# Kernel tuning notes

Hardware: AMD Instinct MI355X
Metric: run time of the kernel (lower is better)

The kernel has to match this reference:

```python
import jax, jax.numpy as jnp
import numpy as np

NUM_ITER = 3
SLOT_DIM = 16
INPUT_DIM = 256
HIDDEN_DIM = 128
EPS = 1e-8
LN_EPS = 1e-5  # torch LayerNorm default


def _layernorm(x, w, b):
    mu = jnp.mean(x, axis=-1, keepdims=True)
    var = jnp.mean((x - mu) ** 2, axis=-1, keepdims=True)
    return (x - mu) * jax.lax.rsqrt(var + LN_EPS) * w + b


def setup_inputs() -> dict:
    key = jax.random.key(0)
    ks = jax.random.split(key, 12)
    B, N, K = 32, 4096, 8
    D, S, H = INPUT_DIM, SLOT_DIM, HIDDEN_DIM
    inputs = jax.random.normal(ks[0], (B, N, D), dtype=jnp.float32)
    init_slots = jax.random.normal(ks[1], (B, K, S), dtype=jnp.float32)
    return {
        "inputs": inputs,
        "init_slots": init_slots,
        "ln_in_w": jnp.ones((D,), jnp.float32),
        "ln_in_b": jnp.zeros((D,), jnp.float32),
        "ln_s_w": jnp.ones((S,), jnp.float32),
        "ln_s_b": jnp.zeros((S,), jnp.float32),
        "ln_m_w": jnp.ones((S,), jnp.float32),
        "ln_m_b": jnp.zeros((S,), jnp.float32),
        "wq": jax.random.normal(ks[2], (S, S), jnp.float32) * (S ** -0.5),
        "wk": jax.random.normal(ks[3], (S, D), jnp.float32) * (D ** -0.5),
        "wv": jax.random.normal(ks[4], (S, D), jnp.float32) * (D ** -0.5),
        "w_ih": jax.random.normal(ks[5], (3 * S, S), jnp.float32) * (S ** -0.5),
        "w_hh": jax.random.normal(ks[6], (3 * S, S), jnp.float32) * (S ** -0.5),
        "b_ih": jnp.zeros((3 * S,), jnp.float32),
        "b_hh": jnp.zeros((3 * S,), jnp.float32),
        "mlp_w1": jax.random.normal(ks[7], (H, S), jnp.float32) * (S ** -0.5),
        "mlp_b1": jnp.zeros((H,), jnp.float32),
        "mlp_w2": jax.random.normal(ks[8], (S, H), jnp.float32) * (H ** -0.5),
        "mlp_b2": jnp.zeros((S,), jnp.float32),
    }


def _gru_cell(x, h, w_ih, w_hh, b_ih, b_hh):
    # torch GRUCell: gates ordered [r, z, n]
    gi = x @ w_ih.T + b_ih            # [BK, 3S]
    gh = h @ w_hh.T + b_hh
    i_r, i_z, i_n = jnp.split(gi, 3, axis=-1)
    h_r, h_z, h_n = jnp.split(gh, 3, axis=-1)
    r = jax.nn.sigmoid(i_r + h_r)
    z = jax.nn.sigmoid(i_z + h_z)
    n = jnp.tanh(i_n + r * h_n)
    return (1.0 - z) * n + z * h


def reference(inputs, init_slots, ln_in_w, ln_in_b, ln_s_w, ln_s_b, ln_m_w, ln_m_b,
              wq, wk, wv, w_ih, w_hh, b_ih, b_hh, mlp_w1, mlp_b1, mlp_w2, mlp_b2):
    B, N, _ = inputs.shape
    K = init_slots.shape[1]
    scale = SLOT_DIM ** -0.5

    x = _layernorm(inputs, ln_in_w, ln_in_b)
    k = jnp.einsum('bnd,sd->bns', x, wk)   # [B,N,S]
    v = jnp.einsum('bnd,sd->bns', x, wv)

    slots = init_slots
    attn = None
    for _ in range(NUM_ITER):
        slots_prev = slots
        q = jnp.einsum('bks,ts->bkt', _layernorm(slots, ln_s_w, ln_s_b), wq)
        logits = jnp.einsum('bks,bns->bkn', q, k) * scale       # [B,K,N]
        attn = jax.nn.softmax(logits, axis=1) + EPS              # softmax over SLOTS
        attn = attn / jnp.sum(attn, axis=-1, keepdims=True)
        updates = jnp.einsum('bkn,bns->bks', attn, v)            # [B,K,S]
        h = _gru_cell(updates.reshape(B * K, -1), slots_prev.reshape(B * K, -1),
                      w_ih, w_hh, b_ih, b_hh).reshape(B, K, -1)
        y = _layernorm(h, ln_m_w, ln_m_b)
        mlp = jax.nn.relu(y @ mlp_w1.T + mlp_b1) @ mlp_w2.T + mlp_b2
        slots = h + mlp
    return slots, attn
```

## Files before the change

kernel.cpp:

```cpp
#include <hip/hip_runtime.h>
#include <cstddef>


typedef unsigned short ushort_t;
typedef __attribute__((ext_vector_type(8))) short short8;
typedef __attribute__((ext_vector_type(4))) float f32x4;

__device__ __forceinline__ float sigmoid_f(float x){ return 1.f/(1.f+__expf(-x)); }
__device__ __forceinline__ float tanh_f(float x){ return 1.f - 2.f/(__expf(2.f*x)+1.f); }

__device__ __forceinline__ ushort_t f2bf(float x){
  unsigned u = __float_as_uint(x);
  return (ushort_t)((u + 0x7FFFu + ((u>>16)&1u)) >> 16);
}
__device__ __forceinline__ float bf2f(ushort_t b){
  return __uint_as_float(((unsigned)b) << 16);
}
__device__ __forceinline__ void split_bf(float v, short& hi, short& lo){
  unsigned u = __float_as_uint(v);
  hi = (short)(u >> 16);
  float hf = __uint_as_float(u & 0xFFFF0000u);
  lo = (short)(__float_as_uint(v - hf) >> 16);
}

__device__ __forceinline__ unsigned ld_cohpt(const unsigned* p){
  unsigned v;
  asm volatile("global_load_dword %0, %1, off sc0 sc1\n\t"
               "s_waitcnt vmcnt(0)"
               : "=v"(v) : "v"(p) : "memory");
  return v;
}
__device__ __forceinline__ void st_agent(float* p, float v){
  __hip_atomic_store(p, v, __ATOMIC_RELAXED, __HIP_MEMORY_SCOPE_AGENT);
}
__device__ __forceinline__ float ld_agent(const float* p){
  return __hip_atomic_load(p, __ATOMIC_RELAXED, __HIP_MEMORY_SCOPE_AGENT);
}

#define VT_OFF    0
#define QS_OFF    16896
#define SLOTS_OFF 17408
#define APART_OFF 17920
#define ULDS_OFF  18048
#define MT_OFF    18560
#define X_OFF     18816
#define KLDS_OFF  (X_OFF + 33792)
#define PT_OFF    X_OFF
#define GW_OFF    (X_OFF + 8448)
#define SMEM_BYTES (X_OFF + 51200)

__global__ __launch_bounds__(256, 2) void k_mega(
    const float* __restrict__ x,
    const float* __restrict__ wk, const float* __restrict__ wv,
    const float* __restrict__ lnw, const float* __restrict__ lnb,
    const float* __restrict__ init_slots,
    float* __restrict__ updp, float* __restrict__ Asum,
    unsigned* __restrict__ barp,
    float* __restrict__ slots_out, float* __restrict__ attn_out,
    const float* __restrict__ w_ih, const float* __restrict__ w_hh,
    const float* __restrict__ b_ih, const float* __restrict__ b_hh,
    const float* __restrict__ mlp_w1, const float* __restrict__ mlp_b1,
    const float* __restrict__ mlp_w2, const float* __restrict__ mlp_b2,
    const float* __restrict__ ln_m_w, const float* __restrict__ ln_m_b,
    const float* __restrict__ ln_s_w, const float* __restrict__ ln_s_b,
    const float* __restrict__ wq)
{
  __shared__ __align__(16) unsigned char smem[SMEM_BYTES];
  ushort_t* vt     = (ushort_t*)(smem + VT_OFF);
  float*    qs     = (float*)(smem + QS_OFF);
  float*    sslots = (float*)(smem + SLOTS_OFF);
  float*    apart  = (float*)(smem + APART_OFF);
  float*    ulds   = (float*)(smem + ULDS_OFF);
  float*    mtf    = (float*)(smem + MT_OFF);
  ushort_t* wlds   = (ushort_t*)(smem + X_OFF);
  float*    klds   = (float*)(smem + KLDS_OFF);
  ushort_t* pt     = (ushort_t*)(smem + PT_OFF);
  float*    s_wih  = (float*)(smem + GW_OFF);
  float*    s_whh  = s_wih + 48*17;
  float*    s_w1   = s_whh + 48*17;
  float*    s_w2   = s_w1 + 128*17;
  float*    s_bih  = s_w2 + 16*129;
  float*    s_bhh  = s_bih + 48;
  float*    s_b1   = s_bhh + 48;
  float*    s_b2   = s_b1 + 128;
  float*    s_lnmw = s_b2 + 16;
  float*    s_lnmb = s_lnmw + 16;
  float*    s_lnsw = s_lnmb + 16;
  float*    s_lnsb = s_lnsw + 16;
  float*    s_wq   = s_lnsb + 16;

  int t = threadIdx.x;
  int lane = t & 63;
  int w = t >> 6;
  int b  = blockIdx.x >> 4;
  int nc = blockIdx.x & 15;
  int n0 = nc << 8;

  {
    unsigned* dst = (unsigned*)wlds;
    #pragma unroll
    for (int i0 = 0; i0 < 8192; i0 += 256) {
      int i = i0 + t;
      int r = i >> 7, ww = i & 127;
      int s = (r & 31);
      int d = ww*2;
      float wa = (s < 16) ? wk[s*256+d]   : wv[(s-16)*256+d];
      float wb = (s < 16) ? wk[s*256+d+1] : wv[(s-16)*256+d+1];
      float w0a = lnw[d]*wa, w0b = lnw[d+1]*wb;
      ushort_t ha = f2bf(w0a), hb2 = f2bf(w0b);
      unsigned word;
      if (r < 32) {
        word = (unsigned)ha | ((unsigned)hb2 << 16);
      } else {
        ushort_t la = f2bf(w0a - bf2f(ha));
        ushort_t lb = f2bf(w0b - bf2f(hb2));
        word = (unsigned)la | ((unsigned)lb << 16);
      }
      dst[r*132 + ww] = word;
    }
  }
  {
    int s = t >> 3, j = t & 7;
    float m = 0.f, tv = 0.f;
    for (int d = j; d < 256; d += 8) {
      float w_ = (s < 16) ? wk[s*256+d] : wv[(s-16)*256+d];
      float w0 = lnw[d]*w_;
      ushort_t hb = f2bf(w0);
      float hf = bf2f(hb);
      float lf = bf2f(f2bf(w0 - hf));
      m  += hf + lf;
      tv  = fmaf(lnb[d], w_, tv);
    }
    m += __shfl_xor(m,1);  m += __shfl_xor(m,2);  m += __shfl_xor(m,4);
    tv += __shfl_xor(tv,1); tv += __shfl_xor(tv,2); tv += __shfl_xor(tv,4);
    if (j == 0) { mtf[s] = m; mtf[32+s] = tv; }
  }
  if (t < 8) {
    float sl[16];
    #pragma unroll
    for (int j2 = 0; j2 < 16; ++j2) sl[j2] = init_slots[(b*8+t)*16+j2];
    float mu = 0.f;
    #pragma unroll
    for (int j2 = 0; j2 < 16; ++j2) mu += sl[j2];
    mu *= (1.f/16.f);
    float var = 0.f;
    #pragma unroll
    for (int j2 = 0; j2 < 16; ++j2) { float d = sl[j2]-mu; var = fmaf(d,d,var); }
    var *= (1.f/16.f);
    float rstd = rsqrtf(var + 1e-5f);
    float y[16];
    #pragma unroll
    for (int j2 = 0; j2 < 16; ++j2) y[j2] = (sl[j2]-mu)*rstd*ln_s_w[j2] + ln_s_b[j2];
    #pragma unroll
    for (int tq = 0; tq < 16; ++tq) {
      float q = 0.f;
      #pragma unroll
      for (int s2 = 0; s2 < 16; ++s2) q = fmaf(y[s2], wq[tq*16+s2], q);
      qs[t*16+tq] = q;
    }
  }
  if (t < 128) sslots[t] = init_slots[b*128 + t];
  __syncthreads();

  int m = lane & 15, quad = lane >> 4;
  const ushort_t* rhk = wlds + (size_t)m*264 + quad*8;
  const ushort_t* rhv = wlds + (size_t)(16+m)*264 + quad*8;
  const ushort_t* rlk = wlds + (size_t)(32+m)*264 + quad*8;
  const ushort_t* rlv = wlds + (size_t)(48+m)*264 + quad*8;
  float mtk  = mtf[m],    mtv  = mtf[16+m];
  float mtkb = mtf[32+m], mtvb = mtf[48+m];

  #pragma unroll
  for (int tile = 0; tile < 4; ++tile) {
    const float* xr = x + (size_t)(b*4096 + n0 + tile*64 + w*16 + m)*256 + quad*8;
    float4 xreg[16];
    #pragma unroll
    for (int kk = 0; kk < 8; ++kk) {
      xreg[2*kk]   = *(const float4*)(xr + kk*32);
      xreg[2*kk+1] = *(const float4*)(xr + kk*32 + 4);
    }
    f32x4 acck = {0.f,0.f,0.f,0.f}, accv = {0.f,0.f,0.f,0.f};
    float sum = 0.f, sumsq = 0.f;
    #pragma unroll
    for (int kk = 0; kk < 8; ++kk) {
      short8 bh_k = *(const short8*)(rhk + kk*32);
      short8 bh_v = *(const short8*)(rhv + kk*32);
      short8 bl_k = *(const short8*)(rlk + kk*32);
      short8 bl_v = *(const short8*)(rlv + kk*32);
      float xv[8] = {xreg[2*kk].x, xreg[2*kk].y, xreg[2*kk].z, xreg[2*kk].w,
                     xreg[2*kk+1].x, xreg[2*kk+1].y, xreg[2*kk+1].z, xreg[2*kk+1].w};
      short8 ah, al;
      #pragma unroll
      for (int j = 0; j < 8; ++j) {
        float v = xv[j];
        sum += v; sumsq = fmaf(v, v, sumsq);
        short h_, l_;
        split_bf(v, h_, l_);
        ah[j] = h_; al[j] = l_;
      }
      acck = __builtin_amdgcn_mfma_f32_16x16x32_bf16(ah, bh_k, acck, 0, 0, 0);
      accv = __builtin_amdgcn_mfma_f32_16x16x32_bf16(ah, bh_v, accv, 0, 0, 0);
      acck = __builtin_amdgcn_mfma_f32_16x16x32_bf16(al, bh_k, acck, 0, 0, 0);
      accv = __builtin_amdgcn_mfma_f32_16x16x32_bf16(al, bh_v, accv, 0, 0, 0);
      acck = __builtin_amdgcn_mfma_f32_16x16x32_bf16(ah, bl_k, acck, 0, 0, 0);
      accv = __builtin_amdgcn_mfma_f32_16x16x32_bf16(ah, bl_v, accv, 0, 0, 0);
    }
    sum   += __shfl_xor(sum, 16);   sum   += __shfl_xor(sum, 32);
    sumsq += __shfl_xor(sumsq, 16); sumsq += __shfl_xor(sumsq, 32);
    #pragma unroll
    for (int r = 0; r < 4; ++r) {
      int row = quad*4 + r;
      float s_ = __shfl(sum,   row);
      float q_ = __shfl(sumsq, row);
      float mu = s_*(1.f/256.f);
      float var = q_*(1.f/256.f) - mu*mu;
      float rstd = rsqrtf(var + 1e-5f);
      float ok = fmaf(rstd, acck[r] - mu*mtk, mtkb);
      float ov = fmaf(rstd, accv[r] - mu*mtv, mtvb);
      int gr = tile*64 + w*16 + row;
      klds[gr*17 + m] = ok;
      short h_, l_;
      split_bf(ov, h_, l_);
      vt[m*264 + gr]      = (ushort_t)h_;
      vt[(16+m)*264 + gr] = (ushort_t)l_;
    }
  }
  __syncthreads();
  float kv[16];
  #pragma unroll
  for (int j = 0; j < 16; ++j) kv[j] = klds[t*17 + j];
  __syncthreads();

  for (int i = t; i < 768; i += 256) {
    int g = i >> 4, j = i & 15;
    s_wih[g*17+j] = w_ih[i];
    s_whh[g*17+j] = w_hh[i];
  }
  for (int i = t; i < 2048; i += 256) {
    int r = i >> 4, c = i & 15;
    s_w1[r*17+c] = mlp_w1[i];
    int r2 = i >> 7, c2 = i & 127;
    s_w2[r2*129+c2] = mlp_w2[i];
  }
  if (t < 48) { s_bih[t] = b_ih[t]; s_bhh[t] = b_hh[t]; }
  if (t < 128) s_b1[t] = mlp_b1[t];
  if (t < 16) {
    s_b2[t] = mlp_b2[t];
    s_lnmw[t] = ln_m_w[t]; s_lnmb[t] = ln_m_b[t];
    s_lnsw[t] = ln_s_w[t]; s_lnsb[t] = ln_s_b[t];
  }
  for (int i = t; i < 256; i += 256) {
    int r = i >> 4, c = i & 15;
    s_wq[r*17+c] = wq[i];
  }
  __syncthreads();

  const short8 z8 = {0,0,0,0,0,0,0,0};
  #pragma unroll 1
  for (int it = 0; it < 3; ++it) {
    float* upd_it = updp + (size_t)(it*32 + b)*2048;
    float* As_it  = Asum + (size_t)(it*32 + b)*128;

    float p8[8];
    {
      float lg[8];
      #pragma unroll
      for (int kk = 0; kk < 8; ++kk) {
        float a = 0.f;
        #pragma unroll
        for (int s = 0; s < 16; ++s) a = fmaf(qs[kk*16+s], kv[s], a);
        lg[kk] = a*0.25f;
      }
      float mx = lg[0];
      #pragma unroll
      for (int kk = 1; kk < 8; ++kk) mx = fmaxf(mx, lg[kk]);
      float se = 0.f;
      #pragma unroll
      for (int kk = 0; kk < 8; ++kk) { lg[kk] = __expf(lg[kk]-mx); se += lg[kk]; }
      float inv = 1.f/se;
      #pragma unroll
      for (int kk = 0; kk < 8; ++kk) p8[kk] = fmaf(lg[kk], inv, 1e-8f);
    }
    #pragma unroll
    for (int kk = 0; kk < 8; ++kk) {
      float r = p8[kk];
      r += __shfl_xor(r, 1);  r += __shfl_xor(r, 2);  r += __shfl_xor(r, 4);
      r += __shfl_xor(r, 8);  r += __shfl_xor(r, 16); r += __shfl_xor(r, 32);
      if (lane == 0) apart[w*8 + kk] = r;
    }
    #pragma unroll
    for (int kk = 0; kk < 8; ++kk) {
      short h_, l_;
      split_bf(p8[kk], h_, l_);
      pt[kk*264 + t]     = (ushort_t)h_;
      pt[(8+kk)*264 + t] = (ushort_t)l_;
    }
    __syncthreads();
    if (t < 8)
      st_agent(As_it + nc*8 + t,
               apart[t] + apart[8+t] + apart[16+t] + apart[24+t]);
    if (w == 0) {
      int mm = lane & 15, q2 = lane >> 4;
      f32x4 acc = {0.f,0.f,0.f,0.f};
      #pragma unroll
      for (int c = 0; c < 8; ++c) {
        int k0 = c*32 + q2*8;
        short8 ah = (mm < 8) ? *(const short8*)&pt[mm*264 + k0]     : z8;
        short8 al = (mm < 8) ? *(const short8*)&pt[(8+mm)*264 + k0] : z8;
        short8 bh = *(const short8*)&vt[mm*264 + k0];
        short8 bl = *(const short8*)&vt[(16+mm)*264 + k0];
        acc = __builtin_amdgcn_mfma_f32_16x16x32_bf16(ah, bh, acc, 0, 0, 0);
        acc = __builtin_amdgcn_mfma_f32_16x16x32_bf16(al, bh, acc, 0, 0, 0);
        acc = __builtin_amdgcn_mfma_f32_16x16x32_bf16(ah, bl, acc, 0, 0, 0);
      }
      int s = lane & 15;
      #pragma unroll
      for (int r = 0; r < 4; ++r) {
        int kk = q2*4 + r;
        if (kk < 8) st_agent(upd_it + nc*128 + kk*16 + s, acc[r]);
      }
    }

    __syncthreads();
    if (t == 0) {
      unsigned* bp = barp + (it*32 + b)*32;
      asm volatile("s_waitcnt vmcnt(0)" ::: "memory");
      atomicAdd(bp, 1u);
      #pragma unroll 1
      for (int spin = 0; spin < (1<<18); ++spin) {
        if (ld_cohpt(bp) >= 16u) break;
        __builtin_amdgcn_s_sleep(8);
      }
    }
    __syncthreads();

    if (t < 8) {
      float a = 0.f;
      #pragma unroll
      for (int nc2 = 0; nc2 < 16; ++nc2) a += ld_agent(As_it + nc2*8 + t);
      apart[t] = a;
    }
    if (t < 128) {
      int bk8 = t >> 4, s = t & 15;
      float us = 0.f;
      #pragma unroll
      for (int nc2 = 0; nc2 < 16; ++nc2)
        us += ld_agent(upd_it + nc2*128 + bk8*16 + s);
      ulds[t] = us;
    }
    __syncthreads();

    if (it == 2) {
      #pragma unroll
      for (int kk = 0; kk < 8; ++kk)
        attn_out[((size_t)(b*8 + kk))*4096 + n0 + t] = p8[kk]*(1.f/apart[kk]);
    }
    if (t < 128 && (it < 2 || nc == 0)) {
      int bk8 = t >> 4, s = t & 15;
      int laneBase = (t & 63) & ~15;
      float invA = 1.f / apart[bk8];
      float u[16], h[16];
      #pragma unroll
      for (int j = 0; j < 16; ++j) {
        u[j] = ulds[bk8*16 + j] * invA;
        h[j] = sslots[bk8*16 + j];
      }
      float hs = h[s];
      float gir = s_bih[s],  giz = s_bih[16+s], gin = s_bih[32+s];
      float ghr = s_bhh[s],  ghz = s_bhh[16+s], ghn = s_bhh[32+s];
      #pragma unroll
      for (int j = 0; j < 16; ++j) {
        gir = fmaf(u[j], s_wih[s*17+j], gir);
        giz = fmaf(u[j], s_wih[(16+s)*17+j], giz);
        gin = fmaf(u[j], s_wih[(32+s)*17+j], gin);
        ghr = fmaf(h[j], s_whh[s*17+j], ghr);
        ghz = fmaf(h[j], s_whh[(16+s)*17+j], ghz);
        ghn = fmaf(h[j], s_whh[(32+s)*17+j], ghn);
      }
      float rr_ = sigmoid_f(gir + ghr);
      float zz = sigmoid_f(giz + ghz);
      float nn = tanh_f(gin + rr_*ghn);
      float hn = (1.f - zz)*nn + zz*hs;

      float ssum = hn;
      #pragma unroll
      for (int mm = 1; mm < 16; mm <<= 1) ssum += __shfl_xor(ssum, mm);
      float mu = ssum*(1.f/16.f);
      float dv = hn - mu;
      float vs = dv*dv;
      #pragma unroll
      for (int mm = 1; mm < 16; mm <<= 1) vs += __shfl_xor(vs, mm);
      float rstd = rsqrtf(vs*(1.f/16.f) + 1e-5f);
      float y = dv*rstd*s_lnmw[s] + s_lnmb[s];

      float yv[16];
      #pragma unroll
      for (int j = 0; j < 16; ++j) yv[j] = __shfl(y, laneBase + j);

      float h1[8];
      #pragma unroll
      for (int i = 0; i < 8; ++i) {
        int jj = i*16 + s;
        float a = s_b1[jj];
        #pragma unroll
        for (int q = 0; q < 16; ++q) a = fmaf(yv[q], s_w1[jj*17+q], a);
        h1[i] = fmaxf(a, 0.f);
      }
      float o = s_b2[s];
      #pragma unroll
      for (int i = 0; i < 8; ++i) {
        #pragma unroll
        for (int sp = 0; sp < 16; ++sp) {
          float hv = __shfl(h1[i], laneBase + sp);
          o = fmaf(hv, s_w2[s*129 + i*16 + sp], o);
        }
      }
      float slot_new = hn + o;
      if (it < 2) {
        sslots[bk8*16 + s] = slot_new;
        float ss = slot_new;
        #pragma unroll
        for (int mm = 1; mm < 16; mm <<= 1) ss += __shfl_xor(ss, mm);
        float mu2 = ss*(1.f/16.f);
        float d2 = slot_new - mu2;
        float v2 = d2*d2;
        #pragma unroll
        for (int mm = 1; mm < 16; mm <<= 1) v2 += __shfl_xor(v2, mm);
        float rstd2 = rsqrtf(v2*(1.f/16.f) + 1e-5f);
        float y2 = d2*rstd2*s_lnsw[s] + s_lnsb[s];
        float qv = 0.f;
        #pragma unroll
        for (int sp = 0; sp < 16; ++sp)
          qv = fmaf(__shfl(y2, laneBase + sp), s_wq[s*17+sp], qv);
        qs[bk8*16 + s] = qv;
      } else {
        slots_out[(b*8 + bk8)*16 + s] = slot_new;
      }
    }
    __syncthreads();
  }
}


__global__ __launch_bounds__(256) void k_prep(
    const float* __restrict__ lnw, const float* __restrict__ lnb,
    const float* __restrict__ wk, const float* __restrict__ wv,
    const float* __restrict__ init_slots,
    const float* __restrict__ ln_s_w, const float* __restrict__ ln_s_b,
    const float* __restrict__ wq,
    ushort_t* __restrict__ Wh, ushort_t* __restrict__ Wl,
    float* __restrict__ mt,
    float* __restrict__ qbuf, float* __restrict__ upd, float* __restrict__ Abuf,
    float* __restrict__ slots_out)
{
  int t = threadIdx.x;
  int i = blockIdx.x*256 + t;
  {
    int s = i >> 8, d = i & 255;
    float w = (s < 16) ? wk[s*256+d] : wv[(s-16)*256+d];
    float w0 = lnw[d]*w;
    ushort_t hb = f2bf(w0);
    ushort_t lb = f2bf(w0 - bf2f(hb));
    Wh[i] = hb; Wl[i] = lb;
  }
  if (blockIdx.x != 0) return;
  {
    int s = t >> 3, j = t & 7;
    float m = 0.f, tv = 0.f;
    for (int d = j; d < 256; d += 8) {
      float w = (s < 16) ? wk[s*256+d] : wv[(s-16)*256+d];
      float w0 = lnw[d]*w;
      ushort_t hb = f2bf(w0);
      float hf = bf2f(hb);
      float lf = bf2f(f2bf(w0 - hf));
      m  += hf + lf;
      tv  = fmaf(lnb[d], w, tv);
    }
    m += __shfl_xor(m,1);  m += __shfl_xor(m,2);  m += __shfl_xor(m,4);
    tv += __shfl_xor(tv,1); tv += __shfl_xor(tv,2); tv += __shfl_xor(tv,4);
    if (j == 0) { mt[s] = m; mt[32+s] = tv; }
  }
  #pragma unroll
  for (int j2 = 0; j2 < 16; ++j2) {
    slots_out[t*16+j2] = init_slots[t*16+j2];
    upd[t*16+j2] = 0.f;
  }
  Abuf[t] = 0.f;
  float sl[16];
  #pragma unroll
  for (int j2 = 0; j2 < 16; ++j2) sl[j2] = init_slots[t*16+j2];
  float mu = 0.f;
  #pragma unroll
  for (int j2 = 0; j2 < 16; ++j2) mu += sl[j2];
  mu *= (1.f/16.f);
  float var = 0.f;
  #pragma unroll
  for (int j2 = 0; j2 < 16; ++j2) { float d = sl[j2]-mu; var = fmaf(d,d,var); }
  var *= (1.f/16.f);
  float rstd = rsqrtf(var + 1e-5f);
  float y[16];
  #pragma unroll
  for (int j2 = 0; j2 < 16; ++j2) y[j2] = (sl[j2]-mu)*rstd*ln_s_w[j2] + ln_s_b[j2];
  #pragma unroll
  for (int tq = 0; tq < 16; ++tq) {
    float q = 0.f;
    #pragma unroll
    for (int s2 = 0; s2 < 16; ++s2) q = fmaf(y[s2], wq[tq*16+s2], q);
    qbuf[t*16+tq] = q;
  }
}

__global__ __launch_bounds__(256, 4) void k_proj(
    const float* __restrict__ x, const ushort_t* __restrict__ Wh,
    const ushort_t* __restrict__ Wl, const float* __restrict__ mt,
    float* __restrict__ kout, float* __restrict__ vout)
{
  __shared__ ushort_t wlds[64*264];
  int t = threadIdx.x;
  int lane = t & 63;
  int p = __builtin_amdgcn_readfirstlane(t >> 6);
  int m = lane & 15, quad = lane >> 4;
  int r0 = blockIdx.x*64;
  {
    const unsigned* srcH = (const unsigned*)Wh;
    const unsigned* srcL = (const unsigned*)Wl;
    unsigned* dst = (unsigned*)wlds;
    #pragma unroll
    for (int i0 = 0; i0 < 8192; i0 += 256) {
      int i = i0 + t;
      int r = i >> 7, w = i & 127;
      unsigned v = (r < 32) ? srcH[r*128 + w] : srcL[(r-32)*128 + w];
      dst[r*132 + w] = v;
    }
  }
  __syncthreads();

  const ushort_t* rhk = wlds + (size_t)m*264 + quad*8;
  const ushort_t* rhv = wlds + (size_t)(16+m)*264 + quad*8;
  const ushort_t* rlk = wlds + (size_t)(32+m)*264 + quad*8;
  const ushort_t* rlv = wlds + (size_t)(48+m)*264 + quad*8;

  const float* xr = x + (size_t)(r0 + p*16 + m)*256 + quad*8;

  f32x4 acck = {0.f,0.f,0.f,0.f}, accv = {0.f,0.f,0.f,0.f};
  float sum = 0.f, sumsq = 0.f;

  #pragma unroll
  for (int kk = 0; kk < 8; ++kk) {
    float4 a0 = *(const float4*)(xr + kk*32);
    float4 a1 = *(const float4*)(xr + kk*32 + 4);
    short8 bh_k = *(const short8*)(rhk + kk*32);
    short8 bh_v = *(const short8*)(rhv + kk*32);
    short8 bl_k = *(const short8*)(rlk + kk*32);
    short8 bl_v = *(const short8*)(rlv + kk*32);
    float xv[8] = {a0.x,a0.y,a0.z,a0.w, a1.x,a1.y,a1.z,a1.w};
    short8 ah, al;
    #pragma unroll
    for (int j = 0; j < 8; ++j) {
      float v = xv[j];
      sum += v; sumsq = fmaf(v, v, sumsq);
      short h_, l_;
      split_bf(v, h_, l_);
      ah[j] = h_; al[j] = l_;
    }
    acck = __builtin_amdgcn_mfma_f32_16x16x32_bf16(ah, bh_k, acck, 0, 0, 0);
    accv = __builtin_amdgcn_mfma_f32_16x16x32_bf16(ah, bh_v, accv, 0, 0, 0);
    acck = __builtin_amdgcn_mfma_f32_16x16x32_bf16(al, bh_k, acck, 0, 0, 0);
    accv = __builtin_amdgcn_mfma_f32_16x16x32_bf16(al, bh_v, accv, 0, 0, 0);
    acck = __builtin_amdgcn_mfma_f32_16x16x32_bf16(ah, bl_k, acck, 0, 0, 0);
    accv = __builtin_amdgcn_mfma_f32_16x16x32_bf16(ah, bl_v, accv, 0, 0, 0);
  }

  sum   += __shfl_xor(sum, 16);  sum   += __shfl_xor(sum, 32);
  sumsq += __shfl_xor(sumsq, 16); sumsq += __shfl_xor(sumsq, 32);

  float mtk  = mt[m],    mtv  = mt[16+m];
  float mtkb = mt[32+m], mtvb = mt[48+m];
  #pragma unroll
  for (int r = 0; r < 4; ++r) {
    int row = quad*4 + r;
    float s_ = __shfl(sum,   row);
    float q_ = __shfl(sumsq, row);
    float mu = s_*(1.f/256.f);
    float var = q_*(1.f/256.f) - mu*mu;
    float rstd = rsqrtf(var + 1e-5f);
    float ok = fmaf(rstd, acck[r] - mu*mtk, mtkb);
    float ov = fmaf(rstd, accv[r] - mu*mtv, mtvb);
    size_t grow = (size_t)(r0 + p*16 + row)*16 + m;
    kout[grow] = ok;
    vout[grow] = ov;
  }
}

__global__ __launch_bounds__(256) void k_attn(
    const float* __restrict__ kproj, const float* __restrict__ vproj,
    const float* __restrict__ qbuf,
    float* __restrict__ upd, float* __restrict__ Abuf,
    float* __restrict__ attn_out, int write_attn)
{
  __shared__ ushort_t vt[32*264];
  __shared__ ushort_t pt[32*264];
  __shared__ float qs[128];
  __shared__ float apart[4][8];
  int b = blockIdx.x >> 4;
  int n0 = (blockIdx.x & 15) * 256;
  int t = threadIdx.x;
  int w = t >> 6, lane = t & 63;

  if (t < 128) qs[t] = qbuf[b*128 + t];

  const float* kr = kproj + ((size_t)(b*4096 + n0 + t))*16;
  const float* vr = vproj + ((size_t)(b*4096 + n0 + t))*16;
  float kv[16], vv[16];
  #pragma unroll
  for (int j = 0; j < 16; j += 4) {
    float4 f = *(const float4*)(kr+j);
    kv[j]=f.x; kv[j+1]=f.y; kv[j+2]=f.z; kv[j+3]=f.w;
    float4 g = *(const float4*)(vr+j);
    vv[j]=g.x; vv[j+1]=g.y; vv[j+2]=g.z; vv[j+3]=g.w;
  }
  #pragma unroll
  for (int s = 0; s < 16; ++s) {
    short h_, l_;
    split_bf(vv[s], h_, l_);
    vt[s*264 + t] = (ushort_t)h_;
    vt[(16+s)*264 + t] = (ushort_t)l_;
  }
  __syncthreads();

  float p8[8];
  {
    float lg[8];
    #pragma unroll
    for (int kk = 0; kk < 8; ++kk) {
      float a = 0.f;
      #pragma unroll
      for (int s = 0; s < 16; ++s) a = fmaf(qs[kk*16+s], kv[s], a);
      lg[kk] = a*0.25f;
    }
    float mx = lg[0];
    #pragma unroll
    for (int kk = 1; kk < 8; ++kk) mx = fmaxf(mx, lg[kk]);
    float se = 0.f;
    #pragma unroll
    for (int kk = 0; kk < 8; ++kk) { lg[kk] = __expf(lg[kk]-mx); se += lg[kk]; }
    float inv = 1.f/se;
    #pragma unroll
    for (int kk = 0; kk < 8; ++kk) {
      float pv = fmaf(lg[kk], inv, 1e-8f);
      p8[kk] = pv;
      if (write_attn) attn_out[((size_t)(b*8+kk))*4096 + n0 + t] = pv;
    }
  }
  #pragma unroll
  for (int kk = 0; kk < 8; ++kk) {
    float r = p8[kk];
    r += __shfl_xor(r, 1);  r += __shfl_xor(r, 2);  r += __shfl_xor(r, 4);
    r += __shfl_xor(r, 8);  r += __shfl_xor(r, 16); r += __shfl_xor(r, 32);
    if (lane == 0) apart[w][kk] = r;
  }
  #pragma unroll
  for (int kk = 0; kk < 8; ++kk) {
    short h_, l_;
    split_bf(p8[kk], h_, l_);
    pt[kk*264 + t] = (ushort_t)h_;
    pt[(16+kk)*264 + t] = (ushort_t)l_;
  }
  __syncthreads();

  if (t < 8)
    atomicAdd(Abuf + b*8 + t,
              apart[0][t] + apart[1][t] + apart[2][t] + apart[3][t]);

  if (w == 0) {
    int mm = lane & 15, quad = lane >> 4;
// ... 169 lines not shown
__global__ __launch_bounds__(256) void k_final(
    float* __restrict__ upd, float* __restrict__ Abuf,
    float* __restrict__ slots, float* __restrict__ qbuf,
    float* __restrict__ attn,
    const float* __restrict__ w_ih, const float* __restrict__ w_hh,
    const float* __restrict__ b_ih, const float* __restrict__ b_hh,
    const float* __restrict__ mlp_w1, const float* __restrict__ mlp_b1,
    const float* __restrict__ mlp_w2, const float* __restrict__ mlp_b2,
    const float* __restrict__ ln_m_w, const float* __restrict__ ln_m_b,
    const float* __restrict__ ln_s_w, const float* __restrict__ ln_s_b,
    const float* __restrict__ wq)
{
  int t = threadIdx.x;
  {
    int bk = blockIdx.x;
    float inv = 1.f / Abuf[bk];
    float4* p = (float4*)(attn + (size_t)bk*4096);
    #pragma unroll 4
    for (int i = t; i < 1024; i += 256) {
      float4 v = p[i];
      v.x *= inv; v.y *= inv; v.z *= inv; v.w *= inv;
      p[i] = v;
    }
  }
  if (blockIdx.x >= 16) return;
  GRU_STAGE_LDS()
  int bk = blockIdx.x*16 + (t >> 4);
  int s = t & 15;
  int laneBase = (t & 63) & ~15;
  gru_body(bk, s, laneBase, 0, upd, Abuf, slots, qbuf,
           s_wih, s_whh, s_bih, s_bhh, s_w1, s_b1, s_w2, s_b2,
           s_lnmw, s_lnmb, s_lnsw, s_lnsb, s_wq);
}

extern "C" void kernel_launch(void* const* d_in, const int* in_sizes, int n_in,
                              void* d_out, int out_size, void* d_ws, size_t ws_size,
                              hipStream_t stream)
{
  const float* inputs     = (const float*)d_in[0];
  const float* init_slots = (const float*)d_in[1];
  const float* ln_in_w    = (const float*)d_in[2];
  const float* ln_in_b    = (const float*)d_in[3];
  const float* ln_s_w     = (const float*)d_in[4];
  const float* ln_s_b     = (const float*)d_in[5];
  const float* ln_m_w     = (const float*)d_in[6];
  const float* ln_m_b     = (const float*)d_in[7];
  const float* wq         = (const float*)d_in[8];
  const float* wk         = (const float*)d_in[9];
  const float* wv         = (const float*)d_in[10];
  const float* w_ih       = (const float*)d_in[11];
  const float* w_hh       = (const float*)d_in[12];
  const float* b_ih       = (const float*)d_in[13];
  const float* b_hh       = (const float*)d_in[14];
  const float* mlp_w1     = (const float*)d_in[15];
  const float* mlp_b1     = (const float*)d_in[16];
  const float* mlp_w2     = (const float*)d_in[17];
  const float* mlp_b2     = (const float*)d_in[18];

  float* ws = (float*)d_ws;
  unsigned* barp = (unsigned*)ws;
  float* updp = ws + 3072;
  float* Asum = ws + 3072 + 196608;
  float* lg    = ws + 211968;
  ushort_t* Wh = (ushort_t*)lg;
  ushort_t* Wl = (ushort_t*)(lg + 4096);
  float* mt    = lg + 8192;
  float* qbuf  = lg + 8320;
  float* upd   = lg + 12416;
  float* Abuf  = lg + 16512;
  float* kproj = lg + 16768;
  float* vproj = kproj + 2097152;

  float* out   = (float*)d_out;
  float* slots = out;
  float* attn  = out + 4096;

  static int s_mode = -1;
  if (s_mode < 0) {
    int dev = 0;
    (void)hipGetDevice(&dev);
    int ncu = 0;
    (void)hipDeviceGetAttribute(&ncu, hipDeviceAttributeMultiprocessorCount, dev);
    int nb = 0;
    if (hipOccupancyMaxActiveBlocksPerMultiprocessor(&nb, (const void*)k_mega,
                                                     256, 0) != hipSuccess)
      nb = 0;
    s_mode = (nb > 0 && ncu > 0 && (long)nb * ncu >= 512) ? 0 : 1;
  }

  if (s_mode == 0) {
    (void)hipMemsetAsync(barp, 0, 3*32*32*sizeof(unsigned), stream);
    k_mega<<<512, 256, 0, stream>>>(inputs, wk, wv, ln_in_w, ln_in_b,
                                    init_slots, updp, Asum, barp, slots, attn,
                                    w_ih, w_hh, b_ih, b_hh,
                                    mlp_w1, mlp_b1, mlp_w2, mlp_b2,
                                    ln_m_w, ln_m_b, ln_s_w, ln_s_b, wq);
    return;
  }

  {
    (void)hipMemsetAsync(barp, 0, 3*32*32*sizeof(unsigned), stream);
    void* kargs[] = {
      (void*)&inputs, (void*)&wk, (void*)&wv, (void*)&ln_in_w, (void*)&ln_in_b,
      (void*)&init_slots, (void*)&updp, (void*)&Asum, (void*)&barp,
      (void*)&slots, (void*)&attn, (void*)&w_ih, (void*)&w_hh,
      (void*)&b_ih, (void*)&b_hh, (void*)&mlp_w1, (void*)&mlp_b1,
      (void*)&mlp_w2, (void*)&mlp_b2, (void*)&ln_m_w, (void*)&ln_m_b,
      (void*)&ln_s_w, (void*)&ln_s_b, (void*)&wq };
    hipError_t err = hipLaunchCooperativeKernel((const void*)k_mega,
                                                dim3(512), dim3(256),
                                                kargs, 0, stream);
    if (err == hipSuccess) return;
    (void)hipGetLastError();
  }

  k_prep<<<32, 256, 0, stream>>>(ln_in_w, ln_in_b, wk, wv, init_slots,
                                 ln_s_w, ln_s_b, wq,
                                 Wh, Wl, mt, qbuf, upd, Abuf, slots);
  k_proj<<<2048, 256, 0, stream>>>(inputs, Wh, Wl, mt, kproj, vproj);
  for (int it = 0; it < 3; ++it) {
    int last = (it == 2);
    k_attn<<<512, 256, 0, stream>>>(kproj, vproj, qbuf, upd, Abuf, attn, last);
    if (!last)
      k_gru<<<16, 256, 0, stream>>>(upd, Abuf, slots, qbuf,
                                    w_ih, w_hh, b_ih, b_hh,
                                    mlp_w1, mlp_b1, mlp_w2, mlp_b2,
                                    ln_m_w, ln_m_b, ln_s_w, ln_s_b, wq);
  }
  k_final<<<256, 256, 0, stream>>>(upd, Abuf, slots, qbuf, attn,
                                   w_ih, w_hh, b_ih, b_hh,
                                   mlp_w1, mlp_b1, mlp_w2, mlp_b2,
                                   ln_m_w, ln_m_b, ln_s_w, ln_s_b, wq);
}
```

Baseline: 307.9 us.

## Split projection out of persistent megakernel into separate prep and proj kernels

The persistent megakernel no longer computes the LayerNorm plus K/V projection itself. Separate k_prep and k_proj kernels now run first, and a slimmer k_iter kernel reads the projected K/V back from global memory, with less LDS per block so three blocks fit per CU instead of two. The barrier memset is folded into k_prep, and the spin timeout is shortened. This trades an extra round trip of K/V through global memory and an extra launch for better occupancy and full-GPU parallelism on the projection.

New measurement: 324.8 us. 1.05x slower.

```diff
diff --git a/kernel.cpp b/kernel.cpp
--- a/kernel.cpp
+++ b/kernel.cpp
@@ -37,23 +37,170 @@
   return __hip_atomic_load(p, __ATOMIC_RELAXED, __HIP_MEMORY_SCOPE_AGENT);
 }
 
-#define VT_OFF    0
-#define QS_OFF    16896
-#define SLOTS_OFF 17408
-#define APART_OFF 17920
-#define ULDS_OFF  18048
-#define MT_OFF    18560
-#define X_OFF     18816
-#define KLDS_OFF  (X_OFF + 33792)
-#define PT_OFF    X_OFF
-#define GW_OFF    (X_OFF + 8448)
-#define SMEM_BYTES (X_OFF + 51200)
-
-__global__ __launch_bounds__(256, 2) void k_mega(
-    const float* __restrict__ x,
+__global__ __launch_bounds__(256) void k_prep(
+    const float* __restrict__ lnw, const float* __restrict__ lnb,
     const float* __restrict__ wk, const float* __restrict__ wv,
-    const float* __restrict__ lnw, const float* __restrict__ lnb,
     const float* __restrict__ init_slots,
+    const float* __restrict__ ln_s_w, const float* __restrict__ ln_s_b,
+    const float* __restrict__ wq,
+    ushort_t* __restrict__ Wh, ushort_t* __restrict__ Wl,
+    float* __restrict__ mt,
+    float* __restrict__ qbuf, float* __restrict__ upd, float* __restrict__ Abuf,
+    unsigned* __restrict__ barp,
+    float* __restrict__ slots_out)
+{
+  int t = threadIdx.x;
+  int i = blockIdx.x*256 + t;
+  {
+    int s = i >> 8, d = i & 255;
+    float w = (s < 16) ? wk[s*256+d] : wv[(s-16)*256+d];
+    float w0 = lnw[d]*w;
+    ushort_t hb = f2bf(w0);
+    ushort_t lb = f2bf(w0 - bf2f(hb));
+    Wh[i] = hb; Wl[i] = lb;
+  }
+  if (blockIdx.x != 0) return;
+  {
+    int s = t >> 3, j = t & 7;
+    float m = 0.f, tv = 0.f;
+    for (int d = j; d < 256; d += 8) {
+      float w = (s < 16) ? wk[s*256+d] : wv[(s-16)*256+d];
+      float w0 = lnw[d]*w;
+      ushort_t hb = f2bf(w0);
+      float hf = bf2f(hb);
+      float lf = bf2f(f2bf(w0 - hf));
+      m  += hf + lf;
+      tv  = fmaf(lnb[d], w, tv);
+    }
+    m += __shfl_xor(m,1);  m += __shfl_xor(m,2);  m += __shfl_xor(m,4);
+    tv += __shfl_xor(tv,1); tv += __shfl_xor(tv,2); tv += __shfl_xor(tv,4);
+    if (j == 0) { mt[s] = m; mt[32+s] = tv; }
+  }
+  #pragma unroll
+  for (int j2 = 0; j2 < 16; ++j2) {
+    slots_out[t*16+j2] = init_slots[t*16+j2];
+    upd[t*16+j2] = 0.f;
+  }
+  Abuf[t] = 0.f;
+  for (int i2 = t; i2 < 3072; i2 += 256) barp[i2] = 0u;
+  float sl[16];
+  #pragma unroll
+  for (int j2 = 0; j2 < 16; ++j2) sl[j2] = init_slots[t*16+j2];
+  float mu = 0.f;
+  #pragma unroll
+  for (int j2 = 0; j2 < 16; ++j2) mu += sl[j2];
+  mu *= (1.f/16.f);
+  float var = 0.f;
+  #pragma unroll
+  for (int j2 = 0; j2 < 16; ++j2) { float d = sl[j2]-mu; var = fmaf(d,d,var); }
+  var *= (1.f/16.f);
+  float rstd = rsqrtf(var + 1e-5f);
+  float y[16];
+  #pragma unroll
+  for (int j2 = 0; j2 < 16; ++j2) y[j2] = (sl[j2]-mu)*rstd*ln_s_w[j2] + ln_s_b[j2];
+  #pragma unroll
+  for (int tq = 0; tq < 16; ++tq) {
+    float q = 0.f;
+    #pragma unroll
+    for (int s2 = 0; s2 < 16; ++s2) q = fmaf(y[s2], wq[tq*16+s2], q);
+    qbuf[t*16+tq] = q;
+  }
+}
+
+__global__ __launch_bounds__(256, 4) void k_proj(
+    const float* __restrict__ x, const ushort_t* __restrict__ Wh,
+    const ushort_t* __restrict__ Wl, const float* __restrict__ mt,
+    float* __restrict__ kout, float* __restrict__ vout)
+{
+  __shared__ ushort_t wlds[64*264];
+  int t = threadIdx.x;
+  int lane = t & 63;
+  int p = __builtin_amdgcn_readfirstlane(t >> 6);
+  int m = lane & 15, quad = lane >> 4;
+  int r0 = blockIdx.x*64;
+  {
+    const unsigned* srcH = (const unsigned*)Wh;
+    const unsigned* srcL = (const unsigned*)Wl;
+    unsigned* dst = (unsigned*)wlds;
+    #pragma unroll
+    for (int i0 = 0; i0 < 8192; i0 += 256) {
+      int i = i0 + t;
+      int r = i >> 7, w = i & 127;
+      unsigned v = (r < 32) ? srcH[r*128 + w] : srcL[(r-32)*128 + w];
+      dst[r*132 + w] = v;
+    }
+  }
+  __syncthreads();
+
+  const ushort_t* rhk = wlds + (size_t)m*264 + quad*8;
+  const ushort_t* rhv = wlds + (size_t)(16+m)*264 + quad*8;
+  const ushort_t* rlk = wlds + (size_t)(32+m)*264 + quad*8;
+  const ushort_t* rlv = wlds + (size_t)(48+m)*264 + quad*8;
+
+  const float* xr = x + (size_t)(r0 + p*16 + m)*256 + quad*8;
+
+  f32x4 acck = {0.f,0.f,0.f,0.f}, accv = {0.f,0.f,0.f,0.f};
+  float sum = 0.f, sumsq = 0.f;
+
+  #pragma unroll
+  for (int kk = 0; kk < 8; ++kk) {
+    float4 a0 = *(const float4*)(xr + kk*32);
+    float4 a1 = *(const float4*)(xr + kk*32 + 4);
+    short8 bh_k = *(const short8*)(rhk + kk*32);
+    short8 bh_v = *(const short8*)(rhv + kk*32);
+    short8 bl_k = *(const short8*)(rlk + kk*32);
+    short8 bl_v = *(const short8*)(rlv + kk*32);
+    float xv[8] = {a0.x,a0.y,a0.z,a0.w, a1.x,a1.y,a1.z,a1.w};
+    short8 ah, al;
+    #pragma unroll
+    for (int j = 0; j < 8; ++j) {
+      float v = xv[j];
+      sum += v; sumsq = fmaf(v, v, sumsq);
+      short h_, l_;
+      split_bf(v, h_, l_);
+      ah[j] = h_; al[j] = l_;
+    }
+    acck = __builtin_amdgcn_mfma_f32_16x16x32_bf16(ah, bh_k, acck, 0, 0, 0);
+    accv = __builtin_amdgcn_mfma_f32_16x16x32_bf16(ah, bh_v, accv, 0, 0, 0);
+    acck = __builtin_amdgcn_mfma_f32_16x16x32_bf16(al, bh_k, acck, 0, 0, 0);
+    accv = __builtin_amdgcn_mfma_f32_16x16x32_bf16(al, bh_v, accv, 0, 0, 0);
+    acck = __builtin_amdgcn_mfma_f32_16x16x32_bf16(ah, bl_k, acck, 0, 0, 0);
+    accv = __builtin_amdgcn_mfma_f32_16x16x32_bf16(ah, bl_v, accv, 0, 0, 0);
+  }
+
+  sum   += __shfl_xor(sum, 16);  sum   += __shfl_xor(sum, 32);
+  sumsq += __shfl_xor(sumsq, 16); sumsq += __shfl_xor(sumsq, 32);
+
+  float mtk  = mt[m],    mtv  = mt[16+m];
+  float mtkb = mt[32+m], mtvb = mt[48+m];
+  #pragma unroll
+  for (int r = 0; r < 4; ++r) {
+    int row = quad*4 + r;
+    float s_ = __shfl(sum,   row);
+    float q_ = __shfl(sumsq, row);
+    float mu = s_*(1.f/256.f);
+    float var = q_*(1.f/256.f) - mu*mu;
+    float rstd = rsqrtf(var + 1e-5f);
+    float ok = fmaf(rstd, acck[r] - mu*mtk, mtkb);
+    float ov = fmaf(rstd, accv[r] - mu*mtv, mtvb);
+    size_t grow = (size_t)(r0 + p*16 + row)*16 + m;
+    kout[grow] = ok;
+    vout[grow] = ov;
+  }
+}
+
+#define IT_VT 0
+#define IT_PT 16896
+#define IT_QS 25344
+#define IT_SL 25856
+#define IT_AP 26368
+#define IT_UL 26496
+#define IT_GW 27008
+#define IT_BYTES 52800
+
+__global__ __launch_bounds__(256, 3) void k_iter(
+    const float* __restrict__ kproj, const float* __restrict__ vproj,
+    const float* __restrict__ qbuf, const float* __restrict__ init_slots,
     float* __restrict__ updp, float* __restrict__ Asum,
     unsigned* __restrict__ barp,
     float* __restrict__ slots_out, float* __restrict__ attn_out,
@@ -65,17 +212,14 @@
     const float* __restrict__ ln_s_w, const float* __restrict__ ln_s_b,
     const float* __restrict__ wq)
 {
-  __shared__ __align__(16) unsigned char smem[SMEM_BYTES];
-  ushort_t* vt     = (ushort_t*)(smem + VT_OFF);
-  float*    qs     = (float*)(smem + QS_OFF);
-  float*    sslots = (float*)(smem + SLOTS_OFF);
-  float*    apart  = (float*)(smem + APART_OFF);
-  float*    ulds   = (float*)(smem + ULDS_OFF);
-  float*    mtf    = (float*)(smem + MT_OFF);
-  ushort_t* wlds   = (ushort_t*)(smem + X_OFF);
-  float*    klds   = (float*)(smem + KLDS_OFF);
-  ushort_t* pt     = (ushort_t*)(smem + PT_OFF);
-  float*    s_wih  = (float*)(smem + GW_OFF);
+  __shared__ __align__(16) unsigned char smem[IT_BYTES];
+  ushort_t* vt     = (ushort_t*)(smem + IT_VT);
+  ushort_t* pt     = (ushort_t*)(smem + IT_PT);
+  float*    qs     = (float*)(smem + IT_QS);
+  float*    sslots = (float*)(smem + IT_SL);
+  float*    apart  = (float*)(smem + IT_AP);
+  float*    ulds   = (float*)(smem + IT_UL);
+  float*    s_wih  = (float*)(smem + IT_GW);
   float*    s_whh  = s_wih + 48*17;
   float*    s_w1   = s_whh + 48*17;
   float*    s_w2   = s_w1 + 128*17;
@@ -96,141 +240,23 @@
   int nc = blockIdx.x & 15;
   int n0 = nc << 8;
 
-  {
-    unsigned* dst = (unsigned*)wlds;
-    #pragma unroll
-    for (int i0 = 0; i0 < 8192; i0 += 256) {
-      int i = i0 + t;
-      int r = i >> 7, ww = i & 127;
-      int s = (r & 31);
-      int d = ww*2;
-      float wa = (s < 16) ? wk[s*256+d]   : wv[(s-16)*256+d];
-      float wb = (s < 16) ? wk[s*256+d+1] : wv[(s-16)*256+d+1];
-      float w0a = lnw[d]*wa, w0b = lnw[d+1]*wb;
-      ushort_t ha = f2bf(w0a), hb2 = f2bf(w0b);
-      unsigned word;
-      if (r < 32) {
-        word = (unsigned)ha | ((unsigned)hb2 << 16);
-      } else {
-        ushort_t la = f2bf(w0a - bf2f(ha));
-        ushort_t lb = f2bf(w0b - bf2f(hb2));
-        word = (unsigned)la | ((unsigned)lb << 16);
-      }
-      dst[r*132 + ww] = word;
-    }
-  }
-  {
-    int s = t >> 3, j = t & 7;
-    float m = 0.f, tv = 0.f;
-    for (int d = j; d < 256; d += 8) {
-      float w_ = (s < 16) ? wk[s*256+d] : wv[(s-16)*256+d];
-      float w0 = lnw[d]*w_;
-      ushort_t hb = f2bf(w0);
-      float hf = bf2f(hb);
-      float lf = bf2f(f2bf(w0 - hf));
-      m  += hf + lf;
-      tv  = fmaf(lnb[d], w_, tv);
-    }
-    m += __shfl_xor(m,1);  m += __shfl_xor(m,2);  m += __shfl_xor(m,4);
-    tv += __shfl_xor(tv,1); tv += __shfl_xor(tv,2); tv += __shfl_xor(tv,4);
-    if (j == 0) { mtf[s] = m; mtf[32+s] = tv; }
-  }
-  if (t < 8) {
-    float sl[16];
-    #pragma unroll
-    for (int j2 = 0; j2 < 16; ++j2) sl[j2] = init_slots[(b*8+t)*16+j2];
-    float mu = 0.f;
-    #pragma unroll
-    for (int j2 = 0; j2 < 16; ++j2) mu += sl[j2];
-    mu *= (1.f/16.f);
-    float var = 0.f;
-    #pragma unroll
-    for (int j2 = 0; j2 < 16; ++j2) { float d = sl[j2]-mu; var = fmaf(d,d,var); }
-    var *= (1.f/16.f);
-    float rstd = rsqrtf(var + 1e-5f);
-    float y[16];
-    #pragma unroll
-    for (int j2 = 0; j2 < 16; ++j2) y[j2] = (sl[j2]-mu)*rstd*ln_s_w[j2] + ln_s_b[j2];
-    #pragma unroll
-    for (int tq = 0; tq < 16; ++tq) {
-      float q = 0.f;
-      #pragma unroll
-      for (int s2 = 0; s2 < 16; ++s2) q = fmaf(y[s2], wq[tq*16+s2], q);
-      qs[t*16+tq] = q;
-    }
-  }
-  if (t < 128) sslots[t] = init_slots[b*128 + t];
-  __syncthreads();
-
-  int m = lane & 15, quad = lane >> 4;
-  const ushort_t* rhk = wlds + (size_t)m*264 + quad*8;
-  const ushort_t* rhv = wlds + (size_t)(16+m)*264 + quad*8;
-  const ushort_t* rlk = wlds + (size_t)(32+m)*264 + quad*8;
-  const ushort_t* rlv = wlds + (size_t)(48+m)*264 + quad*8;
-  float mtk  = mtf[m],    mtv  = mtf[16+m];
-  float mtkb = mtf[32+m], mtvb = mtf[48+m];
-
-  #pragma unroll
-  for (int tile = 0; tile < 4; ++tile) {
-    const float* xr = x + (size_t)(b*4096 + n0 + tile*64 + w*16 + m)*256 + quad*8;
-    float4 xreg[16];
-    #pragma unroll
-    for (int kk = 0; kk < 8; ++kk) {
-      xreg[2*kk]   = *(const float4*)(xr + kk*32);
-      xreg[2*kk+1] = *(const float4*)(xr + kk*32 + 4);
-    }
-    f32x4 acck = {0.f,0.f,0.f,0.f}, accv = {0.f,0.f,0.f,0.f};
-    float sum = 0.f, sumsq = 0.f;
-    #pragma unroll
-    for (int kk = 0; kk < 8; ++kk) {
-      short8 bh_k = *(const short8*)(rhk + kk*32);
-      short8 bh_v = *(const short8*)(rhv + kk*32);
-      short8 bl_k = *(const short8*)(rlk + kk*32);
-      short8 bl_v = *(const short8*)(rlv + kk*32);
-      float xv[8] = {xreg[2*kk].x, xreg[2*kk].y, xreg[2*kk].z, xreg[2*kk].w,
-                     xreg[2*kk+1].x, xreg[2*kk+1].y, xreg[2*kk+1].z, xreg[2*kk+1].w};
-      short8 ah, al;
-      #pragma unroll
-      for (int j = 0; j < 8; ++j) {
-        float v = xv[j];
-        sum += v; sumsq = fmaf(v, v, sumsq);
-        short h_, l_;
-        split_bf(v, h_, l_);
-        ah[j] = h_; al[j] = l_;
-      }
-      acck = __builtin_amdgcn_mfma_f32_16x16x32_bf16(ah, bh_k, acck, 0, 0, 0);
-      accv = __builtin_amdgcn_mfma_f32_16x16x32_bf16(ah, bh_v, accv, 0, 0, 0);
-      acck = __builtin_amdgcn_mfma_f32_16x16x32_bf16(al, bh_k, acck, 0, 0, 0);
-      accv = __builtin_amdgcn_mfma_f32_16x16x32_bf16(al, bh_v, accv, 0, 0, 0);
-      acck = __builtin_amdgcn_mfma_f32_16x16x32_bf16(ah, bl_k, acck, 0, 0, 0);
-      accv = __builtin_amdgcn_mfma_f32_16x16x32_bf16(ah, bl_v, accv, 0, 0, 0);
-    }
-    sum   += __shfl_xor(sum, 16);   sum   += __shfl_xor(sum, 32);
-    sumsq += __shfl_xor(sumsq, 16); sumsq += __shfl_xor(sumsq, 32);
-    #pragma unroll
-    for (int r = 0; r < 4; ++r) {
-      int row = quad*4 + r;
-      float s_ = __shfl(sum,   row);
-      float q_ = __shfl(sumsq, row);
-      float mu = s_*(1.f/256.f);
-      float var = q_*(1.f/256.f) - mu*mu;
-      float rstd = rsqrtf(var + 1e-5f);
-      float ok = fmaf(rstd, acck[r] - mu*mtk, mtkb);
-      float ov = fmaf(rstd, accv[r] - mu*mtv, mtvb);
-      int gr = tile*64 + w*16 + row;
-      klds[gr*17 + m] = ok;
-      short h_, l_;
-      split_bf(ov, h_, l_);
-      vt[m*264 + gr]      = (ushort_t)h_;
-      vt[(16+m)*264 + gr] = (ushort_t)l_;
-    }
-  }
-  __syncthreads();
-  float kv[16];
-  #pragma unroll
-  for (int j = 0; j < 16; ++j) kv[j] = klds[t*17 + j];
-  __syncthreads();
-
+  const float* kr = kproj + ((size_t)(b*4096 + n0 + t))*16;
+  const float* vr = vproj + ((size_t)(b*4096 + n0 + t))*16;
+  float kv[16], vv[16];
+  #pragma unroll
+  for (int j = 0; j < 16; j += 4) {
+    float4 f = *(const float4*)(kr+j);
+    kv[j]=f.x; kv[j+1]=f.y; kv[j+2]=f.z; kv[j+3]=f.w;
+    float4 g = *(const float4*)(vr+j);
+    vv[j]=g.x; vv[j+1]=g.y; vv[j+2]=g.z; vv[j+3]=g.w;
+  }
+  #pragma unroll
+  for (int s = 0; s < 16; ++s) {
+    short h_, l_;
+    split_bf(vv[s], h_, l_);
+    vt[s*264 + t]      = (ushort_t)h_;
+    vt[(16+s)*264 + t] = (ushort_t)l_;
+  }
   for (int i = t; i < 768; i += 256) {
     int g = i >> 4, j = i & 15;
     s_wih[g*17+j] = w_ih[i];
@@ -252,6 +278,10 @@
   for (int i = t; i < 256; i += 256) {
     int r = i >> 4, c = i & 15;
     s_wq[r*17+c] = wq[i];
+  }
+  if (t < 128) {
+    qs[t]     = qbuf[b*128 + t];
+    sslots[t] = init_slots[b*128 + t];
   }
   __syncthreads();
 
@@ -327,7 +357,7 @@
       asm volatile("s_waitcnt vmcnt(0)" ::: "memory");
       atomicAdd(bp, 1u);
       #pragma unroll 1
-      for (int spin = 0; spin < (1<<18); ++spin) {
+      for (int spin = 0; spin < (1<<16); ++spin) {
         if (ld_cohpt(bp) >= 16u) break;
         __builtin_amdgcn_s_sleep(8);
       }
@@ -441,156 +471,6 @@
   }
 }
 
-
-__global__ __launch_bounds__(256) void k_prep(
-    const float* __restrict__ lnw, const float* __restrict__ lnb,
-    const float* __restrict__ wk, const float* __restrict__ wv,
-    const float* __restrict__ init_slots,
-    const float* __restrict__ ln_s_w, const float* __restrict__ ln_s_b,
-    const float* __restrict__ wq,
-    ushort_t* __restrict__ Wh, ushort_t* __restrict__ Wl,
-    float* __restrict__ mt,
-    float* __restrict__ qbuf, float* __restrict__ upd, float* __restrict__ Abuf,
-    float* __restrict__ slots_out)
-{
-  int t = threadIdx.x;
-  int i = blockIdx.x*256 + t;
-  {
-    int s = i >> 8, d = i & 255;
-    float w = (s < 16) ? wk[s*256+d] : wv[(s-16)*256+d];
-    float w0 = lnw[d]*w;
-    ushort_t hb = f2bf(w0);
-    ushort_t lb = f2bf(w0 - bf2f(hb));
-    Wh[i] = hb; Wl[i] = lb;
-  }
-  if (blockIdx.x != 0) return;
-  {
-    int s = t >> 3, j = t & 7;
-    float m = 0.f, tv = 0.f;
-    for (int d = j; d < 256; d += 8) {
-      float w = (s < 16) ? wk[s*256+d] : wv[(s-16)*256+d];
-      float w0 = lnw[d]*w;
-      ushort_t hb = f2bf(w0);
-      float hf = bf2f(hb);
-      float lf = bf2f(f2bf(w0 - hf));
-      m  += hf + lf;
-      tv  = fmaf(lnb[d], w, tv);
-    }
-    m += __shfl_xor(m,1);  m += __shfl_xor(m,2);  m += __shfl_xor(m,4);
-    tv += __shfl_xor(tv,1); tv += __shfl_xor(tv,2); tv += __shfl_xor(tv,4);
-    if (j == 0) { mt[s] = m; mt[32+s] = tv; }
-  }
-  #pragma unroll
-  for (int j2 = 0; j2 < 16; ++j2) {
-    slots_out[t*16+j2] = init_slots[t*16+j2];
-    upd[t*16+j2] = 0.f;
-  }
-  Abuf[t] = 0.f;
-  float sl[16];
-  #pragma unroll
-  for (int j2 = 0; j2 < 16; ++j2) sl[j2] = init_slots[t*16+j2];
-  float mu = 0.f;
-  #pragma unroll
-  for (int j2 = 0; j2 < 16; ++j2) mu += sl[j2];
-  mu *= (1.f/16.f);
-  float var = 0.f;
-  #pragma unroll
-  for (int j2 = 0; j2 < 16; ++j2) { float d = sl[j2]-mu; var = fmaf(d,d,var); }
-  var *= (1.f/16.f);
-  float rstd = rsqrtf(var + 1e-5f);
-  float y[16];
-  #pragma unroll
-  for (int j2 = 0; j2 < 16; ++j2) y[j2] = (sl[j2]-mu)*rstd*ln_s_w[j2] + ln_s_b[j2];
-  #pragma unroll
-  for (int tq = 0; tq < 16; ++tq) {
-    float q = 0.f;
-    #pragma unroll
-    for (int s2 = 0; s2 < 16; ++s2) q = fmaf(y[s2], wq[tq*16+s2], q);
-    qbuf[t*16+tq] = q;
-  }
-}
-
-__global__ __launch_bounds__(256, 4) void k_proj(
-    const float* __restrict__ x, const ushort_t* __restrict__ Wh,
-    const ushort_t* __restrict__ Wl, const float* __restrict__ mt,
-    float* __restrict__ kout, float* __restrict__ vout)
-{
-  __shared__ ushort_t wlds[64*264];
-  int t = threadIdx.x;
-  int lane = t & 63;
-  int p = __builtin_amdgcn_readfirstlane(t >> 6);
-  int m = lane & 15, quad = lane >> 4;
-  int r0 = blockIdx.x*64;
-  {
-    const unsigned* srcH = (const unsigned*)Wh;
-    const unsigned* srcL = (const unsigned*)Wl;
-    unsigned* dst = (unsigned*)wlds;
-    #pragma unroll
-    for (int i0 = 0; i0 < 8192; i0 += 256) {
-      int i = i0 + t;
-      int r = i >> 7, w = i & 127;
-      unsigned v = (r < 32) ? srcH[r*128 + w] : srcL[(r-32)*128 + w];
-      dst[r*132 + w] = v;
-    }
-  }
-  __syncthreads();
-
-  const ushort_t* rhk = wlds + (size_t)m*264 + quad*8;
-  const ushort_t* rhv = wlds + (size_t)(16+m)*264 + quad*8;
-  const ushort_t* rlk = wlds + (size_t)(32+m)*264 + quad*8;
-  const ushort_t* rlv = wlds + (size_t)(48+m)*264 + quad*8;
-
-  const float* xr = x + (size_t)(r0 + p*16 + m)*256 + quad*8;
-
-  f32x4 acck = {0.f,0.f,0.f,0.f}, accv = {0.f,0.f,0.f,0.f};
-  float sum = 0.f, sumsq = 0.f;
-
-  #pragma unroll
-  for (int kk = 0; kk < 8; ++kk) {
-    float4 a0 = *(const float4*)(xr + kk*32);
-    float4 a1 = *(const float4*)(xr + kk*32 + 4);
-    short8 bh_k = *(const short8*)(rhk + kk*32);
-    short8 bh_v = *(const short8*)(rhv + kk*32);
-    short8 bl_k = *(const short8*)(rlk + kk*32);
-    short8 bl_v = *(const short8*)(rlv + kk*32);
-    float xv[8] = {a0.x,a0.y,a0.z,a0.w, a1.x,a1.y,a1.z,a1.w};
-    short8 ah, al;
-    #pragma unroll
-    for (int j = 0; j < 8; ++j) {
-      float v = xv[j];
-      sum += v; sumsq = fmaf(v, v, sumsq);
-      short h_, l_;
-      split_bf(v, h_, l_);
-      ah[j] = h_; al[j] = l_;
-    }
-    acck = __builtin_amdgcn_mfma_f32_16x16x32_bf16(ah, bh_k, acck, 0, 0, 0);
-    accv = __builtin_amdgcn_mfma_f32_16x16x32_bf16(ah, bh_v, accv, 0, 0, 0);
-    acck = __builtin_amdgcn_mfma_f32_16x16x32_bf16(al, bh_k, acck, 0, 0, 0);
-    accv = __builtin_amdgcn_mfma_f32_16x16x32_bf16(al, bh_v, accv, 0, 0, 0);
-    acck = __builtin_amdgcn_mfma_f32_16x16x32_bf16(ah, bl_k, acck, 0, 0, 0);
-    accv = __builtin_amdgcn_mfma_f32_16x16x32_bf16(ah, bl_v, accv, 0, 0, 0);
-  }
-
-  sum   += __shfl_xor(sum, 16);  sum   += __shfl_xor(sum, 32);
-  sumsq += __shfl_xor(sumsq, 16); sumsq += __shfl_xor(sumsq, 32);
-
-  float mtk  = mt[m],    mtv  = mt[16+m];
-  float mtkb = mt[32+m], mtvb = mt[48+m];
-  #pragma unroll
-  for (int r = 0; r < 4; ++r) {
-    int row = quad*4 + r;
-    float s_ = __shfl(sum,   row);
-    float q_ = __shfl(sumsq, row);
-    float mu = s_*(1.f/256.f);
-    float var = q_*(1.f/256.f) - mu*mu;
-    float rstd = rsqrtf(var + 1e-5f);
-    float ok = fmaf(rstd, acck[r] - mu*mtk, mtkb);
-    float ov = fmaf(rstd, accv[r] - mu*mtv, mtvb);
-    size_t grow = (size_t)(r0 + p*16 + row)*16 + m;
-    kout[grow] = ok;
-    vout[grow] = ov;
-  }
-}
 
 __global__ __launch_bounds__(256) void k_attn(
     const float* __restrict__ kproj, const float* __restrict__ vproj,
@@ -926,16 +806,20 @@
     int ncu = 0;
     (void)hipDeviceGetAttribute(&ncu, hipDeviceAttributeMultiprocessorCount, dev);
     int nb = 0;
-    if (hipOccupancyMaxActiveBlocksPerMultiprocessor(&nb, (const void*)k_mega,
+    if (hipOccupancyMaxActiveBlocksPerMultiprocessor(&nb, (const void*)k_iter,
                                                      256, 0) != hipSuccess)
       nb = 0;
     s_mode = (nb > 0 && ncu > 0 && (long)nb * ncu >= 512) ? 0 : 1;
   }
 
+  k_prep<<<32, 256, 0, stream>>>(ln_in_w, ln_in_b, wk, wv, init_slots,
+                                 ln_s_w, ln_s_b, wq,
+                                 Wh, Wl, mt, qbuf, upd, Abuf, barp, slots);
+  k_proj<<<2048, 256, 0, stream>>>(inputs, Wh, Wl, mt, kproj, vproj);
+
   if (s_mode == 0) {
-    (void)hipMemsetAsync(barp, 0, 3*32*32*sizeof(unsigned), stream);
-    k_mega<<<512, 256, 0, stream>>>(inputs, wk, wv, ln_in_w, ln_in_b,
-                                    init_slots, updp, Asum, barp, slots, attn,
+    k_iter<<<512, 256, 0, stream>>>(kproj, vproj, qbuf, init_slots,
+                                    updp, Asum, barp, slots, attn,
                                     w_ih, w_hh, b_ih, b_hh,
                                     mlp_w1, mlp_b1, mlp_w2, mlp_b2,
                                     ln_m_w, ln_m_b, ln_s_w, ln_s_b, wq);
@@ -943,25 +827,20 @@
   }
 
   {
-    (void)hipMemsetAsync(barp, 0, 3*32*32*sizeof(unsigned), stream);
     void* kargs[] = {
-      (void*)&inputs, (void*)&wk, (void*)&wv, (void*)&ln_in_w, (void*)&ln_in_b,
-      (void*)&init_slots, (void*)&updp, (void*)&Asum, (void*)&barp,
-      (void*)&slots, (void*)&attn, (void*)&w_ih, (void*)&w_hh,
-      (void*)&b_ih, (void*)&b_hh, (void*)&mlp_w1, (void*)&mlp_b1,
-      (void*)&mlp_w2, (void*)&mlp_b2, (void*)&ln_m_w, (void*)&ln_m_b,
-      (void*)&ln_s_w, (void*)&ln_s_b, (void*)&wq };
-    hipError_t err = hipLaunchCooperativeKernel((const void*)k_mega,
+      (void*)&kproj, (void*)&vproj, (void*)&qbuf, (void*)&init_slots,
+      (void*)&updp, (void*)&Asum, (void*)&barp, (void*)&slots, (void*)&attn,
+      (void*)&w_ih, (void*)&w_hh, (void*)&b_ih, (void*)&b_hh,
+      (void*)&mlp_w1, (void*)&mlp_b1, (void*)&mlp_w2, (void*)&mlp_b2,
+      (void*)&ln_m_w, (void*)&ln_m_b, (void*)&ln_s_w, (void*)&ln_s_b,
+      (void*)&wq };
+    hipError_t err = hipLaunchCooperativeKernel((const void*)k_iter,
                                                 dim3(512), dim3(256),
                                                 kargs, 0, stream);
     if (err == hipSuccess) return;
     (void)hipGetLastError();
   }
 
-  k_prep<<<32, 256, 0, stream>>>(ln_in_w, ln_in_b, wk, wv, init_slots,
-                                 ln_s_w, ln_s_b, wq,
-                                 Wh, Wl, mt, qbuf, upd, Abuf, slots);
-  k_proj<<<2048, 256, 0, stream>>>(inputs, Wh, Wl, mt, kproj, vproj);
   for (int it = 0; it < 3; ++it) {
     int last = (it == 2);
     k_attn<<<512, 256, 0, stream>>>(kproj, vproj, qbuf, upd, Abuf, attn, last);
```
